# Kernel optimization log

Hardware: AMD Instinct MI355X
Metric: run time of the kernel (lower is better)

Reference implementation:

```python
import jax, jax.numpy as jnp
import numpy as np

B, S, D, H = 2, 2048, 1024, 16
HD = D // H  # head_dim = 64


def setup_inputs() -> dict:
    key = jax.random.key(0)
    ks = jax.random.split(key, 12)
    s = 1.0 / np.sqrt(D)
    return {
        "query": jax.random.normal(ks[0], (B, S, D), jnp.float32),
        "key": jax.random.normal(ks[1], (B, S, D), jnp.float32),
        "value": jax.random.normal(ks[2], (B, S, D), jnp.float32),
        "attention_mask": jnp.zeros((B, S, S), jnp.float32),
        "WQ_w": jax.random.normal(ks[3], (D, D), jnp.float32) * s,
        "WQ_b": jnp.zeros((D,), jnp.float32),
        "WK_w": jax.random.normal(ks[4], (D, D), jnp.float32) * s,
        "WK_b": jnp.zeros((D,), jnp.float32),
        "WV_w": jax.random.normal(ks[5], (D, D), jnp.float32) * s,
        "WV_b": jnp.zeros((D,), jnp.float32),
        "WO_w": jax.random.normal(ks[6], (D, D), jnp.float32) * s,
        "WO_b": jnp.zeros((D,), jnp.float32),
    }


def _split_heads(x):
    # [B,S,D] -> [B,H,S,HD]
    b, s, _ = x.shape
    return x.reshape(b, s, H, HD).transpose(0, 2, 1, 3)


def reference(query, key, value, attention_mask,
              WQ_w, WQ_b, WK_w, WK_b, WV_w, WV_b, WO_w, WO_b):
    Q = _split_heads(query @ WQ_w.T + WQ_b)   # [B,H,S,HD]
    K = _split_heads(key @ WK_w.T + WK_b)
    V = _split_heads(value @ WV_w.T + WV_b)
    scale = 1.0 / jnp.sqrt(jnp.float32(HD))
    scores = jnp.einsum('bhqd,bhkd->bhqk', Q, K) * scale
    scores = scores + attention_mask[:, None, :, :]
    attn = jax.nn.softmax(scores, axis=-1)    # dropout_prob=0.0 -> identity
    out = jnp.einsum('bhqk,bhkd->bhqd', attn, V)
    out = out.transpose(0, 2, 1, 3).reshape(query.shape[0], -1, D)
    return out @ WO_w.T + WO_b
```

## Files before the change

kernel.cpp:

```cpp
#include <hip/hip_runtime.h>
#include <math.h>


typedef _Float16 h8 __attribute__((ext_vector_type(8)));
typedef _Float16 h4 __attribute__((ext_vector_type(4)));
typedef float f4 __attribute__((ext_vector_type(4)));

#define MFMA16(a, b, c) __builtin_amdgcn_mfma_f32_16x16x32_f16((a), (b), (c), 0, 0, 0)
#define EXP2F(x) __builtin_amdgcn_exp2f(x)

static constexpr int Bn = 2, Sn = 2048, Dn = 1024, Hn = 16, HDn = 64;
static constexpr int Mn = Bn * Sn;
static constexpr int Kn = Dn;
static constexpr int Nn = Dn;
static constexpr int LDP = 72;
static constexpr float LOG2E = 1.4426950408889634f;

__device__ __forceinline__ void gload_lds16(const _Float16* g, _Float16* l) {
  __builtin_amdgcn_global_load_lds(
      (const __attribute__((address_space(1))) unsigned int*)g,
      (__attribute__((address_space(3))) unsigned int*)l, 16, 0, 0);
}

struct CvtJobs {
  const float* src[7];
  _Float16* dst[7];
  int n4[7];
};

__global__ __launch_bounds__(256) void cvt_kernel(CvtJobs j) {
  const int stride = gridDim.x * blockDim.x;
  const int t0 = blockIdx.x * blockDim.x + threadIdx.x;
#pragma unroll
  for (int k = 0; k < 7; ++k) {
    const float4* __restrict__ s = (const float4*)j.src[k];
    h4* __restrict__ d = (h4*)j.dst[k];
    const int n = j.n4[k];
    for (int i = t0; i < n; i += stride) {
      const float4 f = s[i];
      h4 h;
      h[0] = (_Float16)f.x; h[1] = (_Float16)f.y;
      h[2] = (_Float16)f.z; h[3] = (_Float16)f.w;
      d[i] = h;
    }
  }
}

struct QkvArgs {
  const _Float16* X[3];
  const _Float16* W[3];
  const float* bias[3];
  _Float16* out[3];
};

__global__ __launch_bounds__(256) void gemm_qkv(QkvArgs args) {
  const int z = blockIdx.z;
  const _Float16* __restrict__ X = args.X[z];
  const _Float16* __restrict__ W = args.W[z];
  const float* __restrict__ bias = args.bias[z];
  _Float16* __restrict__ out = args.out[z];

  __shared__ _Float16 As[128 * 64];
  __shared__ _Float16 Bs[128 * 64];

  const int t = threadIdx.x;
  const int lane = t & 63, wv = t >> 6;
  const int l15 = lane & 15, quad = lane >> 4;
  const int wm = (wv >> 1) * 64, wn = (wv & 1) * 64;
  const int n0 = blockIdx.x * 128, m0 = blockIdx.y * 128;

  f4 acc[4][4];
#pragma unroll
  for (int i = 0; i < 4; ++i)
#pragma unroll
    for (int j = 0; j < 4; ++j) {
      f4 zz = {0.f, 0.f, 0.f, 0.f};
      acc[i][j] = zz;
    }

  const int srow = lane >> 3, scol = (lane & 7) * 8;

  for (int k0 = 0; k0 < Kn; k0 += 64) {
    __syncthreads();
#pragma unroll
    for (int u = 0; u < 4; ++u) {
      const int s = wv * 4 + u;
      const int row = s * 8 + srow;
      gload_lds16(X + (size_t)(m0 + row) * Kn + k0 + scol, As + s * 512);
      gload_lds16(W + (size_t)(n0 + row) * Kn + k0 + scol, Bs + s * 512);
    }
    __syncthreads();
#pragma unroll
    for (int kk = 0; kk < 64; kk += 32) {
      h8 af[4], bfr[4];
#pragma unroll
      for (int i = 0; i < 4; ++i)
        af[i] = *(const h8*)&As[(wm + i * 16 + l15) * 64 + kk + quad * 8];
#pragma unroll
      for (int j = 0; j < 4; ++j)
        bfr[j] = *(const h8*)&Bs[(wn + j * 16 + l15) * 64 + kk + quad * 8];
#pragma unroll
      for (int i = 0; i < 4; ++i)
#pragma unroll
        for (int j = 0; j < 4; ++j)
          acc[i][j] = MFMA16(af[i], bfr[j], acc[i][j]);
    }
  }

  const float osc = (z == 0) ? (0.125f * LOG2E) : 1.0f;
  if (z != 2) {
#pragma unroll
    for (int j = 0; j < 4; ++j) {
      const int n = n0 + wn + j * 16 + l15;
      const float bvs = bias[n] * osc;
      const int hh = n >> 6, hd = n & 63;
#pragma unroll
      for (int i = 0; i < 4; ++i) {
        const int mb = m0 + wm + i * 16 + quad * 4;
        const int bb = mb >> 11;
#pragma unroll
        for (int r = 0; r < 4; ++r) {
          const int ss = (mb + r) & (Sn - 1);
          out[(((size_t)(bb * Hn + hh)) * Sn + ss) * HDn + hd] =
              (_Float16)(acc[i][j][r] * osc + bvs);
        }
      }
    }
  } else {
#pragma unroll
    for (int j = 0; j < 4; ++j) {
      const int n = n0 + wn + j * 16 + l15;
      const float bv = bias[n];
      const int hh = n >> 6, hd = n & 63;
#pragma unroll
      for (int i = 0; i < 4; ++i) {
        const int mb = m0 + wm + i * 16 + quad * 4;
        const int bb = mb >> 11, ss = mb & (Sn - 1);
        h4 hv;
#pragma unroll
        for (int r = 0; r < 4; ++r) hv[r] = (_Float16)(acc[i][j][r] + bv);
        *(h4*)(out + (((size_t)(bb * Hn + hh)) * HDn + hd) * Sn + ss) = hv;
      }
    }
  }
}

__global__ __launch_bounds__(256) void gemm_o(const _Float16* __restrict__ X,
                                              const _Float16* __restrict__ W,
                                              const float* __restrict__ bias,
                                              float* __restrict__ out) {
  __shared__ _Float16 As[128 * 64];
  __shared__ _Float16 Bs[128 * 64];

  const int t = threadIdx.x;
  const int lane = t & 63, wv = t >> 6;
  const int l15 = lane & 15, quad = lane >> 4;
  const int wm = (wv >> 1) * 64, wn = (wv & 1) * 64;
  const int n0 = blockIdx.x * 128, m0 = blockIdx.y * 128;

  f4 acc[4][4];
#pragma unroll
  for (int i = 0; i < 4; ++i)
#pragma unroll
    for (int j = 0; j < 4; ++j) {
      f4 zz = {0.f, 0.f, 0.f, 0.f};
      acc[i][j] = zz;
    }

  const int srow = lane >> 3, scol = (lane & 7) * 8;

  for (int k0 = 0; k0 < Kn; k0 += 64) {
    __syncthreads();
#pragma unroll
    for (int u = 0; u < 4; ++u) {
      const int s = wv * 4 + u;
      const int row = s * 8 + srow;
      gload_lds16(X + (size_t)(m0 + row) * Kn + k0 + scol, As + s * 512);
      gload_lds16(W + (size_t)(n0 + row) * Kn + k0 + scol, Bs + s * 512);
    }
    __syncthreads();
#pragma unroll
    for (int kk = 0; kk < 64; kk += 32) {
      h8 af[4], bfr[4];
#pragma unroll
      for (int i = 0; i < 4; ++i)
        af[i] = *(const h8*)&As[(wm + i * 16 + l15) * 64 + kk + quad * 8];
#pragma unroll
      for (int j = 0; j < 4; ++j)
        bfr[j] = *(const h8*)&Bs[(wn + j * 16 + l15) * 64 + kk + quad * 8];
#pragma unroll
      for (int i = 0; i < 4; ++i)
#pragma unroll
        for (int j = 0; j < 4; ++j)
          acc[i][j] = MFMA16(af[i], bfr[j], acc[i][j]);
    }
  }

#pragma unroll
  for (int j = 0; j < 4; ++j) {
    const int n = n0 + wn + j * 16 + l15;
    const float bv = bias[n];
#pragma unroll
    for (int i = 0; i < 4; ++i) {
      const int mb = m0 + wm + i * 16 + quad * 4;
#pragma unroll
      for (int r = 0; r < 4; ++r)
        out[(size_t)(mb + r) * Nn + n] = acc[i][j][r] + bv;
    }
  }
}

__global__ __launch_bounds__(512) void attn_kernel(
    const _Float16* __restrict__ Qh,
    const _Float16* __restrict__ Kh,
    const _Float16* __restrict__ Vt,
    const float* __restrict__ mask,
    _Float16* __restrict__ out) {
  __shared__ _Float16 smem[4 * 64 * LDP];
  __shared__ _Float16 Pl[8 * 16 * LDP];

  const int t = threadIdx.x;
  const int w = t >> 6, lane = t & 63;
  const int l15 = lane & 15, quad = lane >> 4;
  const int g = w >> 2;
  const int wq = w & 3;

  const int bh = blockIdx.y;
  const int b = bh >> 4, h = bh & 15;
  const size_t headoff = (size_t)bh * Sn * HDn;
  const _Float16* Qp = Qh + headoff;
  const _Float16* Kp = Kh + headoff;
  const _Float16* Vp = Vt + headoff;

  const int qb = blockIdx.x * 64;
  const int q0 = qb + wq * 16;
  const h8 qf0 = *(const h8*)(Qp + (size_t)(q0 + l15) * HDn + quad * 8);
  const h8 qf1 = *(const h8*)(Qp + (size_t)(q0 + l15) * HDn + 32 + quad * 8);

  const int kbase = g * (Sn / 2);
  const float* mrow = mask + ((size_t)b * Sn + q0 + l15) * Sn + kbase;

  float m_run = -INFINITY, l_part = 0.f;
  f4 o_acc[4];
#pragma unroll
  for (int nt = 0; nt < 4; ++nt) {
    f4 zz = {0.f, 0.f, 0.f, 0.f};
    o_acc[nt] = zz;
  }

  _Float16* Kg = smem + g * (64 * LDP);
  _Float16* Vg = smem + (2 + g) * (64 * LDP);
  _Float16* Pw = &Pl[(w * 16) * LDP];

  const int tg = t & 255;
  const int srow = tg >> 3, sc8 = (tg & 7) * 8;
  const int srow1 = (tg + 256) >> 3, sc81 = ((tg + 256) & 7) * 8;

  constexpr int NT = (Sn / 2) / 64;

  uint4 kreg0, kreg1, vreg0, vreg1;
  float4 mreg[4];
  auto kv_issue = [&](int kt) {
    kreg0 = *(const uint4*)(Kp + (size_t)(kbase + kt * 64 + srow) * HDn + sc8);
    vreg0 = *(const uint4*)(Vp + (size_t)srow * Sn + kbase + kt * 64 + sc8);
    kreg1 = *(const uint4*)(Kp + (size_t)(kbase + kt * 64 + srow1) * HDn + sc81);
    vreg1 = *(const uint4*)(Vp + (size_t)srow1 * Sn + kbase + kt * 64 + sc81);
  };
  auto m_issue = [&](int kt) {
#pragma unroll
    for (int ks = 0; ks < 4; ++ks)
      mreg[ks] = *(const float4*)(mrow + kt * 64 + ks * 16 + quad * 4);
  };

  kv_issue(0);
  m_issue(0);

  for (int kt = 0; kt < NT; ++kt) {
    __syncthreads();
    *(uint4*)&Kg[srow * LDP + sc8] = kreg0;
    *(uint4*)&Vg[srow * LDP + sc8] = vreg0;
    *(uint4*)&Kg[srow1 * LDP + sc81] = kreg1;
    *(uint4*)&Vg[srow1 * LDP + sc81] = vreg1;
    __syncthreads();
    const int nx = (kt + 1 < NT) ? kt + 1 : kt;
    kv_issue(nx);

    f4 s[4];
#pragma unroll
    for (int ks = 0; ks < 4; ++ks) {
      const h8 kf0 = *(const h8*)&Kg[(ks * 16 + l15) * LDP + quad * 8];
      const h8 kf1 = *(const h8*)&Kg[(ks * 16 + l15) * LDP + 32 + quad * 8];
      f4 a = {0.f, 0.f, 0.f, 0.f};
      a = MFMA16(kf0, qf0, a);
      a = MFMA16(kf1, qf1, a);
#pragma unroll
      for (int r = 0; r < 4; ++r)
        s[ks][r] = fmaf(((const float*)&mreg[ks])[r], LOG2E, a[r]);
    }
    m_issue(nx);

    float mx = s[0][0];
#pragma unroll
    for (int ks = 0; ks < 4; ++ks)
#pragma unroll
      for (int r = 0; r < 4; ++r) mx = fmaxf(mx, s[ks][r]);
    mx = fmaxf(mx, __shfl_xor(mx, 16));
    mx = fmaxf(mx, __shfl_xor(mx, 32));
    const float nm = fmaxf(m_run, mx);
    const float alpha = EXP2F(m_run - nm);
    m_run = nm;
    float sm = 0.f;
#pragma unroll
    for (int ks = 0; ks < 4; ++ks)
#pragma unroll
      for (int r = 0; r < 4; ++r) {
        s[ks][r] = EXP2F(s[ks][r] - nm);
        sm += s[ks][r];
      }
    l_part = l_part * alpha + sm;
#pragma unroll
    for (int nt = 0; nt < 4; ++nt)
#pragma unroll
      for (int r = 0; r < 4; ++r) o_acc[nt][r] *= alpha;

#pragma unroll
    for (int ks = 0; ks < 4; ++ks) {
      h4 pv;
#pragma unroll
      for (int r = 0; r < 4; ++r) pv[r] = (_Float16)s[ks][r];
      *(h4*)&Pw[l15 * LDP + ks * 16 + quad * 4] = pv;
    }

#pragma unroll
    for (int kk = 0; kk < 64; kk += 32) {
      const h8 pf = *(const h8*)&Pw[l15 * LDP + kk + quad * 8];
#pragma unroll
      for (int nt = 0; nt < 4; ++nt) {
        const h8 vf = *(const h8*)&Vg[(nt * 16 + l15) * LDP + kk + quad * 8];
        o_acc[nt] = MFMA16(vf, pf, o_acc[nt]);
      }
    }
  }

  l_part += __shfl_xor(l_part, 16);
  l_part += __shfl_xor(l_part, 32);

  __syncthreads();
  float* Uex = (float*)smem;
  float* mex = Uex + 4 * 16 * LDP;
  float* lex = mex + 64;
  if (g == 1) {
#pragma unroll
    for (int nt = 0; nt < 4; ++nt)
      *(f4*)&Uex[wq * 16 * LDP + l15 * LDP + nt * 16 + quad * 4] = o_acc[nt];
    if (quad == 0) {
      mex[wq * 16 + l15] = m_run;
      lex[wq * 16 + l15] = l_part;
    }
  }
  __syncthreads();
  if (g == 0) {
    const float m1 = mex[wq * 16 + l15];
    const float l1 = lex[wq * 16 + l15];
    const float mm = fmaxf(m_run, m1);
    const float f0 = EXP2F(m_run - mm);
    const float f1 = EXP2F(m1 - mm);
    const float rl = 1.0f / (f0 * l_part + f1 * l1);
#pragma unroll
    for (int nt = 0; nt < 4; ++nt) {
      const f4 Ur = *(const f4*)&Uex[wq * 16 * LDP + l15 * LDP + nt * 16 + quad * 4];
      h4 ov;
#pragma unroll
      for (int r = 0; r < 4; ++r)
        ov[r] = (_Float16)((o_acc[nt][r] * f0 + Ur[r] * f1) * rl);
      *(h4*)&Pw[l15 * LDP + nt * 16 + quad * 4] = ov;
    }
    const int qr = lane >> 2;
    const int seg = (lane & 3) * 16;
    _Float16* dst = out + ((size_t)b * Sn + q0 + qr) * Dn + h * 64 + seg;
    *(uint4*)dst = *(const uint4*)&Pw[qr * LDP + seg];
    *(uint4*)(dst + 8) = *(const uint4*)&Pw[qr * LDP + seg + 8];
  }
}

extern "C" void kernel_launch(void* const* d_in, const int* in_sizes, int n_in,
                              void* d_out, int out_size, void* d_ws, size_t ws_size,
                              hipStream_t stream) {
  const float* q = (const float*)d_in[0];
  const float* k = (const float*)d_in[1];
  const float* v = (const float*)d_in[2];
  const float* mask = (const float*)d_in[3];
  const float* WQ = (const float*)d_in[4];
  const float* bQ = (const float*)d_in[5];
  const float* WK = (const float*)d_in[6];
  const float* bK = (const float*)d_in[7];
  const float* WV = (const float*)d_in[8];
  const float* bV = (const float*)d_in[9];
  const float* WO = (const float*)d_in[10];
  const float* bO = (const float*)d_in[11];

  _Float16* ws = (_Float16*)d_ws;
  const size_t MD = (size_t)Mn * Dn;
  const size_t DD = (size_t)Dn * Dn;
  _Float16* qh  = ws;
  _Float16* kh  = ws + MD;
  _Float16* vh  = ws + 2 * MD;
  _Float16* WQh = ws + 3 * MD;
  _Float16* WKh = WQh + DD;
  _Float16* WVh = WKh + DD;
  _Float16* WOh = WVh + DD;
  _Float16* Qh  = ws + 3 * MD + 4 * DD;
  _Float16* Kh  = Qh + MD;
  _Float16* Vt  = Kh + MD;
  _Float16* AO  = qh;

  CvtJobs cj;
  cj.src[0] = q;  cj.dst[0] = qh;  cj.n4[0] = (int)(MD / 4);
  cj.src[1] = k;  cj.dst[1] = kh;  cj.n4[1] = (int)(MD / 4);
  cj.src[2] = v;  cj.dst[2] = vh;  cj.n4[2] = (int)(MD / 4);
  cj.src[3] = WQ; cj.dst[3] = WQh; cj.n4[3] = (int)(DD / 4);
  cj.src[4] = WK; cj.dst[4] = WKh; cj.n4[4] = (int)(DD / 4);
  cj.src[5] = WV; cj.dst[5] = WVh; cj.n4[5] = (int)(DD / 4);
  cj.src[6] = WO; cj.dst[6] = WOh; cj.n4[6] = (int)(DD / 4);
  cvt_kernel<<<1024, 256, 0, stream>>>(cj);

  QkvArgs ga;
  ga.X[0] = qh; ga.W[0] = WQh; ga.bias[0] = bQ; ga.out[0] = Qh;
  ga.X[1] = kh; ga.W[1] = WKh; ga.bias[1] = bK; ga.out[1] = Kh;
  ga.X[2] = vh; ga.W[2] = WVh; ga.bias[2] = bV; ga.out[2] = Vt;
  gemm_qkv<<<dim3(Nn / 128, Mn / 128, 3), 256, 0, stream>>>(ga);

  attn_kernel<<<dim3(Sn / 64, Bn * Hn), 512, 0, stream>>>(Qh, Kh, Vt, mask, AO);

  gemm_o<<<dim3(Nn / 128, Mn / 128), 256, 0, stream>>>(AO, WOh, bO, (float*)d_out);
}
```

Before: 299.4 us.

## Convert mask to fp16, keep P in registers, and apply lazy softmax rescaling

A new pre-pass converts the fp32 mask into fp16 pre-scaled by log2e. The attention kernel then feeds the mask as the MFMA accumulator initializer, which halves the mask traffic the attention kernel reads 16 times per batch. The V tile is stored in LDS with a permuted column order, so the P fragment can be built directly from the score registers with no LDS round-trip for P. The online-softmax rescale is skipped unless the running max grows by more than 8, trading some fp32 headroom for fewer multiplies. The extra kernel still reads the full 32MB fp32 mask once, and fp16 mask precision could matter for very large negative mask values.

After: 305.4 us. +2.0%, slower.

```diff
diff --git a/kernel.cpp b/kernel.cpp
--- a/kernel.cpp
+++ b/kernel.cpp
@@ -46,6 +46,20 @@
   }
 }
 
+__global__ __launch_bounds__(256) void cvt_mask(const float* __restrict__ src,
+                                                _Float16* __restrict__ dst, int n4) {
+  const int stride = gridDim.x * blockDim.x;
+  const float4* __restrict__ s = (const float4*)src;
+  h4* __restrict__ d = (h4*)dst;
+  for (int i = blockIdx.x * blockDim.x + threadIdx.x; i < n4; i += stride) {
+    const float4 f = s[i];
+    h4 h;
+    h[0] = (_Float16)(f.x * LOG2E); h[1] = (_Float16)(f.y * LOG2E);
+    h[2] = (_Float16)(f.z * LOG2E); h[3] = (_Float16)(f.w * LOG2E);
+    d[i] = h;
+  }
+}
+
 struct QkvArgs {
   const _Float16* X[3];
   const _Float16* W[3];
@@ -214,10 +228,9 @@
     const _Float16* __restrict__ Qh,
     const _Float16* __restrict__ Kh,
     const _Float16* __restrict__ Vt,
-    const float* __restrict__ mask,
+    const _Float16* __restrict__ maskh,
     _Float16* __restrict__ out) {
   __shared__ _Float16 smem[4 * 64 * LDP];
-  __shared__ _Float16 Pl[8 * 16 * LDP];
 
   const int t = threadIdx.x;
   const int w = t >> 6, lane = t & 63;
@@ -238,7 +251,7 @@
   const h8 qf1 = *(const h8*)(Qp + (size_t)(q0 + l15) * HDn + 32 + quad * 8);
 
   const int kbase = g * (Sn / 2);
-  const float* mrow = mask + ((size_t)b * Sn + q0 + l15) * Sn + kbase;
+  const _Float16* mrow = maskh + ((size_t)b * Sn + q0 + l15) * Sn + kbase;
 
   float m_run = -INFINITY, l_part = 0.f;
   f4 o_acc[4];
@@ -250,26 +263,27 @@
 
   _Float16* Kg = smem + g * (64 * LDP);
   _Float16* Vg = smem + (2 + g) * (64 * LDP);
-  _Float16* Pw = &Pl[(w * 16) * LDP];
 
   const int tg = t & 255;
   const int srow = tg >> 3, sc8 = (tg & 7) * 8;
-  const int srow1 = (tg + 256) >> 3, sc81 = ((tg + 256) & 7) * 8;
+  const int srow1 = srow + 32;
+  const int a = tg & 7;
+  const int vb = ((a >> 2) & 1) * 32 + (a & 1) * 16 + ((a >> 1) & 1) * 4;
 
   constexpr int NT = (Sn / 2) / 64;
 
   uint4 kreg0, kreg1, vreg0, vreg1;
-  float4 mreg[4];
+  uint2 mreg[4];
   auto kv_issue = [&](int kt) {
     kreg0 = *(const uint4*)(Kp + (size_t)(kbase + kt * 64 + srow) * HDn + sc8);
     vreg0 = *(const uint4*)(Vp + (size_t)srow * Sn + kbase + kt * 64 + sc8);
-    kreg1 = *(const uint4*)(Kp + (size_t)(kbase + kt * 64 + srow1) * HDn + sc81);
-    vreg1 = *(const uint4*)(Vp + (size_t)srow1 * Sn + kbase + kt * 64 + sc81);
+    kreg1 = *(const uint4*)(Kp + (size_t)(kbase + kt * 64 + srow1) * HDn + sc8);
+    vreg1 = *(const uint4*)(Vp + (size_t)srow1 * Sn + kbase + kt * 64 + sc8);
   };
   auto m_issue = [&](int kt) {
 #pragma unroll
     for (int ks = 0; ks < 4; ++ks)
-      mreg[ks] = *(const float4*)(mrow + kt * 64 + ks * 16 + quad * 4);
+      mreg[ks] = *(const uint2*)(mrow + kt * 64 + ks * 16 + quad * 4);
   };
 
   kv_issue(0);
@@ -278,9 +292,11 @@
   for (int kt = 0; kt < NT; ++kt) {
     __syncthreads();
     *(uint4*)&Kg[srow * LDP + sc8] = kreg0;
-    *(uint4*)&Vg[srow * LDP + sc8] = vreg0;
-    *(uint4*)&Kg[srow1 * LDP + sc81] = kreg1;
-    *(uint4*)&Vg[srow1 * LDP + sc81] = vreg1;
+    *(uint4*)&Kg[srow1 * LDP + sc8] = kreg1;
+    *(uint2*)&Vg[srow * LDP + vb] = make_uint2(vreg0.x, vreg0.y);
+    *(uint2*)&Vg[srow * LDP + vb + 8] = make_uint2(vreg0.z, vreg0.w);
+    *(uint2*)&Vg[srow1 * LDP + vb] = make_uint2(vreg1.x, vreg1.y);
+    *(uint2*)&Vg[srow1 * LDP + vb + 8] = make_uint2(vreg1.z, vreg1.w);
     __syncthreads();
     const int nx = (kt + 1 < NT) ? kt + 1 : kt;
     kv_issue(nx);
@@ -288,14 +304,14 @@
     f4 s[4];
 #pragma unroll
     for (int ks = 0; ks < 4; ++ks) {
+      const h4 mh = *(const h4*)&mreg[ks];
+      f4 acc0;
+#pragma unroll
+      for (int r = 0; r < 4; ++r) acc0[r] = (float)mh[r];
       const h8 kf0 = *(const h8*)&Kg[(ks * 16 + l15) * LDP + quad * 8];
       const h8 kf1 = *(const h8*)&Kg[(ks * 16 + l15) * LDP + 32 + quad * 8];
-      f4 a = {0.f, 0.f, 0.f, 0.f};
-      a = MFMA16(kf0, qf0, a);
-      a = MFMA16(kf1, qf1, a);
-#pragma unroll
-      for (int r = 0; r < 4; ++r)
-        s[ks][r] = fmaf(((const float*)&mreg[ks])[r], LOG2E, a[r]);
+      acc0 = MFMA16(kf0, qf0, acc0);
+      s[ks] = MFMA16(kf1, qf1, acc0);
     }
     m_issue(nx);
 
@@ -306,37 +322,36 @@
       for (int r = 0; r < 4; ++r) mx = fmaxf(mx, s[ks][r]);
     mx = fmaxf(mx, __shfl_xor(mx, 16));
     mx = fmaxf(mx, __shfl_xor(mx, 32));
-    const float nm = fmaxf(m_run, mx);
-    const float alpha = EXP2F(m_run - nm);
-    m_run = nm;
+    if (!__all(mx - m_run <= 8.0f)) {
+      const float nm = fmaxf(m_run, mx);
+      const float alpha = EXP2F(m_run - nm);
+      m_run = nm;
+      l_part *= alpha;
+#pragma unroll
+      for (int nt = 0; nt < 4; ++nt)
+#pragma unroll
+        for (int r = 0; r < 4; ++r) o_acc[nt][r] *= alpha;
+    }
     float sm = 0.f;
 #pragma unroll
     for (int ks = 0; ks < 4; ++ks)
 #pragma unroll
       for (int r = 0; r < 4; ++r) {
-        s[ks][r] = EXP2F(s[ks][r] - nm);
+        s[ks][r] = EXP2F(s[ks][r] - m_run);
         sm += s[ks][r];
       }
-    l_part = l_part * alpha + sm;
-#pragma unroll
-    for (int nt = 0; nt < 4; ++nt)
-#pragma unroll
-      for (int r = 0; r < 4; ++r) o_acc[nt][r] *= alpha;
-
-#pragma unroll
-    for (int ks = 0; ks < 4; ++ks) {
-      h4 pv;
-#pragma unroll
-      for (int r = 0; r < 4; ++r) pv[r] = (_Float16)s[ks][r];
-      *(h4*)&Pw[l15 * LDP + ks * 16 + quad * 4] = pv;
-    }
-
-#pragma unroll
-    for (int kk = 0; kk < 64; kk += 32) {
-      const h8 pf = *(const h8*)&Pw[l15 * LDP + kk + quad * 8];
+    l_part += sm;
+
+#pragma unroll
+    for (int c = 0; c < 2; ++c) {
+      h8 pf;
+#pragma unroll
+      for (int r = 0; r < 4; ++r) pf[r] = (_Float16)s[2 * c][r];
+#pragma unroll
+      for (int r = 0; r < 4; ++r) pf[4 + r] = (_Float16)s[2 * c + 1][r];
 #pragma unroll
       for (int nt = 0; nt < 4; ++nt) {
-        const h8 vf = *(const h8*)&Vg[(nt * 16 + l15) * LDP + kk + quad * 8];
+        const h8 vf = *(const h8*)&Vg[(nt * 16 + l15) * LDP + c * 32 + quad * 8];
         o_acc[nt] = MFMA16(vf, pf, o_acc[nt]);
       }
     }
@@ -366,6 +381,7 @@
     const float f0 = EXP2F(m_run - mm);
     const float f1 = EXP2F(m1 - mm);
     const float rl = 1.0f / (f0 * l_part + f1 * l1);
+    _Float16* Ob = smem + 3 * (64 * LDP) + (w * 16) * LDP;
 #pragma unroll
     for (int nt = 0; nt < 4; ++nt) {
       const f4 Ur = *(const f4*)&Uex[wq * 16 * LDP + l15 * LDP + nt * 16 + quad * 4];
@@ -373,13 +389,13 @@
 #pragma unroll
       for (int r = 0; r < 4; ++r)
         ov[r] = (_Float16)((o_acc[nt][r] * f0 + Ur[r] * f1) * rl);
-      *(h4*)&Pw[l15 * LDP + nt * 16 + quad * 4] = ov;
+      *(h4*)&Ob[l15 * LDP + nt * 16 + quad * 4] = ov;
     }
     const int qr = lane >> 2;
     const int seg = (lane & 3) * 16;
     _Float16* dst = out + ((size_t)b * Sn + q0 + qr) * Dn + h * 64 + seg;
-    *(uint4*)dst = *(const uint4*)&Pw[qr * LDP + seg];
-    *(uint4*)(dst + 8) = *(const uint4*)&Pw[qr * LDP + seg + 8];
+    *(uint4*)dst = *(const uint4*)&Ob[qr * LDP + seg];
+    *(uint4*)(dst + 8) = *(const uint4*)&Ob[qr * LDP + seg + 8];
   }
 }
 
@@ -413,6 +429,7 @@
   _Float16* Kh  = Qh + MD;
   _Float16* Vt  = Kh + MD;
   _Float16* AO  = qh;
+  _Float16* Mh  = kh;
 
   CvtJobs cj;
   cj.src[0] = q;  cj.dst[0] = qh;  cj.n4[0] = (int)(MD / 4);
@@ -430,7 +447,9 @@
   ga.X[2] = vh; ga.W[2] = WVh; ga.bias[2] = bV; ga.out[2] = Vt;
   gemm_qkv<<<dim3(Nn / 128, Mn / 128, 3), 256, 0, stream>>>(ga);
 
-  attn_kernel<<<dim3(Sn / 64, Bn * Hn), 512, 0, stream>>>(Qh, Kh, Vt, mask, AO);
+  cvt_mask<<<2048, 256, 0, stream>>>(mask, Mh, (int)((size_t)Bn * Sn * Sn / 4));
+
+  attn_kernel<<<dim3(Sn / 64, Bn * Hn), 512, 0, stream>>>(Qh, Kh, Vt, Mh, AO);
 
   gemm_o<<<dim3(Nn / 128, Mn / 128), 256, 0, stream>>>(AO, WOh, bO, (float*)d_out);
 }
```
